# Kernel optimization log

Hardware: AMD Instinct MI355X
Metric: run time of the kernel (lower is better)

The kernel has to match this reference:

```python
import jax, jax.numpy as jnp
import numpy as np

TEMPERATURE = 0.5   # cfg.LOSS.TEMPERATURE
REG = 0.5           # Sinkhorn entropic regularization
NUM_ITER = 100      # numItermax in forward call
STOP_THR = 1e-9

BS, NUM_CLASSES, DIM = 16384, 1000, 512


def _l2norm(x):
    return x / jnp.linalg.norm(x, axis=-1, keepdims=True)


def setup_inputs() -> dict:
    key = jax.random.key(0)
    k1, k2, k3 = jax.random.split(key, 3)
    features = _l2norm(jax.random.normal(k1, (BS, DIM), jnp.float32))
    text_features = _l2norm(jax.random.normal(k2, (NUM_CLASSES, DIM), jnp.float32))
    ratios = jax.random.uniform(k3, (NUM_CLASSES,), jnp.float32)
    ratios = ratios / ratios.sum()  # class prior, sums to 1
    return {"features": features, "text_features": text_features, "ratios": ratios}


def sinkhorn_knopp(a, b, M, reg):
    """Faithful Sinkhorn-Knopp: u/v scaling loop with NaN/Inf bail-out and
    every-10-iters convergence check, unrolled as a masked lax.scan."""
    dim_a, dim_b = a.shape[0], b.shape[0]
    K = jnp.exp(M / -reg)                 # [dim_a, dim_b]
    Kp = (1.0 / a)[:, None] * K           # [dim_a, dim_b]
    u0 = jnp.ones((dim_a,), M.dtype) / dim_a
    v0 = jnp.ones((dim_b,), M.dtype) / dim_b

    def step(carry, ii):
        u, v, done = carry
        KtU = K.T @ u                     # [dim_b]
        v_new = b / KtU
        u_new = 1.0 / (Kp @ v_new)        # [dim_a]
        bad = (jnp.any(KtU == 0)
               | jnp.any(~jnp.isfinite(u_new))
               | jnp.any(~jnp.isfinite(v_new)))
        # err check (original does it when ii % 10 == 0)
        tmp2 = (u_new @ K) * v_new        # einsum('i,ij,j->j', u, K, v)
        err = jnp.linalg.norm(tmp2 - b)
        converged = ((ii % 10) == 0) & (err < STOP_THR)
        keep_prev = done | bad            # revert to uprev/vprev on bad, freeze after done
        u2 = jnp.where(keep_prev, u, u_new)
        v2 = jnp.where(keep_prev, v, v_new)
        return (u2, v2, done | bad | converged), None

    (u, v, _), _ = jax.lax.scan(step, (u0, v0, jnp.array(False)), jnp.arange(NUM_ITER))
    return u[:, None] * K * v[None, :]


def reference(features, text_features, ratios):
    sim_matrix = (features @ text_features.T) / TEMPERATURE   # [bs, C]
    cost_matrix = 1.0 - sim_matrix
    bs = features.shape[0]
    a = jnp.ones((bs,), features.dtype)       # row marginal (uniform over batch)
    b = ratios * bs                            # column marginal (class ratios)
    plan = sinkhorn_knopp(a, b, sim_matrix / cost_matrix, REG)  # [bs, C]
    return plan
```

## Files before the change

### kernel.cpp

```cpp
#include <hip/hip_runtime.h>
#include <hip/hip_bf16.h>

typedef float   f32x4_t  __attribute__((ext_vector_type(4)));
typedef float   f32x2_t  __attribute__((ext_vector_type(2)));
typedef __bf16  bf16x8_t __attribute__((ext_vector_type(8)));
typedef int     i32x4_t  __attribute__((ext_vector_type(4)));

#define N_ROWS   16384
#define N_COLS   1000
#define N_COLS_P 1024
#define N_DIM    512
#define N_ITER   100
#define PBLK     256
#define PTHR     512
#define RED0     64

__device__ __forceinline__ float ldf_sc1(const float* p) {
    return __hip_atomic_load(p, __ATOMIC_RELAXED, __HIP_MEMORY_SCOPE_AGENT);
}
__device__ __forceinline__ void stf_sc1(float* p, float v) {
    __hip_atomic_store(p, v, __ATOMIC_RELAXED, __HIP_MEMORY_SCOPE_AGENT);
}
__device__ __forceinline__ int ldi_sc1(const int* p) {
    return __hip_atomic_load(p, __ATOMIC_RELAXED, __HIP_MEMORY_SCOPE_AGENT);
}
__device__ __forceinline__ void sti_sc1(int* p, int v) {
    __hip_atomic_store(p, v, __ATOMIC_RELAXED, __HIP_MEMORY_SCOPE_AGENT);
}
__device__ __forceinline__ void st2_sc1(float* p, float a, float b) {
    const unsigned long long u =
        ((unsigned long long)__builtin_bit_cast(unsigned, b) << 32) |
        __builtin_bit_cast(unsigned, a);
    __hip_atomic_store((unsigned long long*)p, u, __ATOMIC_RELAXED,
                       __HIP_MEMORY_SCOPE_AGENT);
}

__device__ __forceinline__ unsigned short f2bf(float f) {
    unsigned int u = __builtin_bit_cast(unsigned int, f);
    u += 0x7FFFu + ((u >> 16) & 1u);
    return (unsigned short)(u >> 16);
}

__device__ __forceinline__ void gridbar(int* bar, int g) {
    __syncthreads();
    if (blockIdx.x == 0) {
        if (threadIdx.x < 64) {
            const int l = threadIdx.x;
            for (;;) {
                int ok = 1;
#pragma unroll
                for (int h = 0; h < 4; ++h) {
                    const int slot = (h << 6) + l;
                    if (slot) ok &= (ldi_sc1(bar + slot) >= g);
                }
                if (__all(ok)) break;
            }
            if (l == 0) sti_sc1(bar + 256, g);
        }
    } else {
        if (threadIdx.x == 0) {
            sti_sc1(bar + (int)blockIdx.x, g);
            while (ldi_sc1(bar + 256) < g) __builtin_amdgcn_s_sleep(2);
        }
    }
    __syncthreads();
}

template <int MODE>
__launch_bounds__(256)
__global__ void k_gemm(const float* __restrict__ F, const float* __restrict__ T,
                       void* __restrict__ Kout, float* __restrict__ cpart,
                       const float* __restrict__ v_com, const float* __restrict__ u_both,
                       const int* __restrict__ flags)
{
    __shared__ unsigned short lA[128 * 72];
    __shared__ unsigned short lB[128 * 72];
    __shared__ float cs_lds[4 * 64];

    const int bm = blockIdx.x;
    const int bn = blockIdx.y;
    const int m0 = bm << 7;
    const int n0 = bn << 7;
    const int t  = threadIdx.x;
    const int lane = t & 63;
    const int wid  = t >> 6;
    const int wr = wid >> 1;
    const int wc = wid & 1;

    f32x4_t acc[4][4];
#pragma unroll
    for (int a = 0; a < 4; ++a)
#pragma unroll
        for (int b = 0; b < 4; ++b)
            acc[a][b] = (f32x4_t){0.f, 0.f, 0.f, 0.f};

    const int srow = t >> 4;
    const int scol = (t & 15) << 2;

    for (int kt = 0; kt < N_DIM; kt += 64) {
#pragma unroll
        for (int r = 0; r < 8; ++r) {
            const int rr = srow + (r << 4);
            const float4 av = *(const float4*)(F + (size_t)(m0 + rr) * N_DIM + kt + scol);
            ushort4 a4; a4.x = f2bf(av.x); a4.y = f2bf(av.y); a4.z = f2bf(av.z); a4.w = f2bf(av.w);
            *(ushort4*)(&lA[rr * 72 + scol]) = a4;
            const int gn = n0 + rr;
            float4 bv = make_float4(0.f, 0.f, 0.f, 0.f);
            if (gn < N_COLS) bv = *(const float4*)(T + (size_t)gn * N_DIM + kt + scol);
            ushort4 b4; b4.x = f2bf(bv.x); b4.y = f2bf(bv.y); b4.z = f2bf(bv.z); b4.w = f2bf(bv.w);
            *(ushort4*)(&lB[rr * 72 + scol]) = b4;
        }
        __syncthreads();
#pragma unroll
        for (int ks = 0; ks < 2; ++ks) {
            bf16x8_t afr[4], bfr[4];
#pragma unroll
            for (int mf = 0; mf < 4; ++mf) {
                const int r = (wr << 6) + (mf << 4) + (lane & 15);
                const int off = r * 72 + (ks << 5) + ((lane >> 4) << 3);
                afr[mf] = __builtin_bit_cast(bf16x8_t, *(const i32x4_t*)(&lA[off]));
            }
#pragma unroll
            for (int nf = 0; nf < 4; ++nf) {
                const int r = (wc << 6) + (nf << 4) + (lane & 15);
                const int off = r * 72 + (ks << 5) + ((lane >> 4) << 3);
                bfr[nf] = __builtin_bit_cast(bf16x8_t, *(const i32x4_t*)(&lB[off]));
            }
#pragma unroll
            for (int mf = 0; mf < 4; ++mf)
#pragma unroll
                for (int nf = 0; nf < 4; ++nf)
                    acc[mf][nf] = __builtin_amdgcn_mfma_f32_16x16x32_bf16(
                        afr[mf], bfr[nf], acc[mf][nf], 0, 0, 0);
        }
        __syncthreads();
    }

    int usel = 2;
    if (MODE == 1) usel = flags[1];
    float csum[4] = {0.f, 0.f, 0.f, 0.f};
#pragma unroll
    for (int mf = 0; mf < 4; ++mf) {
#pragma unroll
        for (int nf = 0; nf < 4; ++nf) {
#pragma unroll
            for (int j = 0; j < 4; ++j) {
                const float d = acc[mf][nf][j];
                const float s = 2.f * d;
                const float M = s / (1.f - s);
                const float kv = __expf(-2.f * M);
                const int grow = m0 + (wr << 6) + (mf << 4) + ((lane >> 4) << 2) + j;
                const int gcol = n0 + (wc << 6) + (nf << 4) + (lane & 15);
                if (MODE == 0) {
                    ((unsigned short*)Kout)[(size_t)grow * N_COLS_P + gcol] =
                        (gcol < N_COLS) ? f2bf(kv) : (unsigned short)0;
                    csum[nf] += kv;
                } else {
                    if (gcol < N_COLS) {
                        const float u = (usel == 2) ? (1.f / 16384.f)
                                                    : u_both[(size_t)usel * N_ROWS + grow];
                        ((float*)Kout)[(size_t)grow * N_COLS + gcol] = u * kv * v_com[gcol];
                    }
                }
            }
        }
    }
    if (MODE == 0) {
#pragma unroll
        for (int nf = 0; nf < 4; ++nf) {
            csum[nf] += __shfl_xor(csum[nf], 16);
            csum[nf] += __shfl_xor(csum[nf], 32);
        }
        if (lane < 16) {
#pragma unroll
            for (int nf = 0; nf < 4; ++nf)
                cs_lds[wid * 64 + (nf << 4) + lane] = csum[nf];
        }
        __syncthreads();
        if (t < 128) {
            const int cw = t >> 6;
            const int c6 = t & 63;
            cpart[(size_t)bm * N_COLS_P + n0 + t] =
                cs_lds[cw * 64 + c6] + cs_lds[(cw + 2) * 64 + c6];
        }
    }
}

__launch_bounds__(128)
__global__ void k_init(const float* __restrict__ cpart, float* __restrict__ ktu0,
                       float* __restrict__ vcom, float* __restrict__ err2,
                       int* __restrict__ flags, int* __restrict__ bar)
{
    const int j = blockIdx.x * 128 + threadIdx.x;
    if (j < N_COLS) {
        float s = 0.f;
        for (int p = 0; p < 128; ++p) s += cpart[(size_t)p * N_COLS_P + j];
        ktu0[j] = s * (1.f / 16384.f);
        vcom[j] = 1.f / 1000.f;
    } else {
        ktu0[j] = 1.f;
        vcom[j] = 0.f;
    }
    if (j <= 256) bar[j] = 0;
    if (j < 64) err2[j] = 0.f;
    if (j == 0) { flags[0] = 0; flags[1] = 2; flags[2] = 0; flags[3] = 0; }
}

__launch_bounds__(PTHR, 2)
__global__ void k_persist(const unsigned short* __restrict__ Kb,
                          const float* __restrict__ ratios,
                          float* __restrict__ ktu,
                          float* __restrict__ utmp,
                          float* __restrict__ vcom,
                          float* __restrict__ partials,
                          float* __restrict__ err2,
                          int* __restrict__ flags,
                          int* __restrict__ bar)
{
    __shared__ float vnew[N_COLS_P];
    __shared__ float wp[8][N_COLS_P];
    __shared__ float wred[8][16];
    __shared__ float errl[16];
    __shared__ int ibc[2];
    const int t = threadIdx.x, lane = t & 63, wid = t >> 6, b = blockIdx.x;
    const int row0 = (b << 6) + (wid << 3);
    const int rb = b - RED0;
    const bool isred = (rb >= 0 && rb < 64);

    unsigned kp[8][8];
#pragma unroll
    for (int r = 0; r < 8; ++r) {
        const unsigned* rp = (const unsigned*)(Kb + (size_t)(row0 + r) * N_COLS_P);
#pragma unroll
        for (int q = 0; q < 8; ++q) kp[r][q] = rp[(q << 6) + lane];
    }
    const float bj0 = (t < N_COLS) ? ratios[t] * 16384.f : 0.f;
    const float bj1 = (t + PTHR < N_COLS) ? ratios[t + PTHR] * 16384.f : 0.f;

    int bar_g = 0;
    int usel = 2;

    for (int ii = 0; ii < N_ITER; ++ii) {
        const int p = ii & 1;
        float* __restrict__ ktu_cur = ktu + p * N_COLS_P;
        float* __restrict__ ktu_nxt = ktu + (1 - p) * N_COLS_P;

        int badl = 0;
        {
            const float v0 = bj0 / ldf_sc1(ktu_cur + t);
            const float v1 = bj1 / ldf_sc1(ktu_cur + t + PTHR);
            badl |= !isfinite(v0) | !isfinite(v1);
            vnew[t] = v0;
            vnew[t + PTHR] = v1;
        }
        __syncthreads();
        float vr[16];
#pragma unroll
        for (int q = 0; q < 8; ++q) {
            const f32x2_t vv = *(const f32x2_t*)&vnew[(q << 7) + (lane << 1)];
            vr[2*q] = vv[0]; vr[2*q+1] = vv[1];
        }
        float dots[8];
#pragma unroll
        for (int r = 0; r < 8; ++r) {
            float p0 = 0.f, p1 = 0.f, p2 = 0.f, p3 = 0.f;
#pragma unroll
            for (int q = 0; q < 8; ++q) {
                const unsigned u = kp[r][q];
                const float lo = __builtin_bit_cast(float, u << 16);
                const float hi = __builtin_bit_cast(float, u & 0xFFFF0000u);
                if (q & 1) { p2 = fmaf(lo, vr[2*q], p2); p3 = fmaf(hi, vr[2*q+1], p3); }
                else       { p0 = fmaf(lo, vr[2*q], p0); p1 = fmaf(hi, vr[2*q+1], p1); }
            }
            dots[r] = (p0 + p1) + (p2 + p3);
        }
#pragma unroll
        for (int s = 1; s <= 32; s <<= 1) {
#pragma unroll
            for (int r = 0; r < 8; ++r) dots[r] += __shfl_xor(dots[r], s);
        }
        float u8[8];
#pragma unroll
        for (int r = 0; r < 8; ++r) { u8[r] = 1.f / dots[r]; badl |= !isfinite(u8[r]); }
        if (lane == 0) {
            float* uo = utmp + (size_t)p * N_ROWS + row0;
#pragma unroll
            for (int r = 0; r < 8; ++r) uo[r] = u8[r];
        }
        if (__any(badl) && lane == 0)
            __hip_atomic_fetch_or(&flags[2], 1, __ATOMIC_RELAXED, __HIP_MEMORY_SCOPE_AGENT);

        float creg[16];
#pragma unroll
        for (int e = 0; e < 16; ++e) creg[e] = 0.f;
#pragma unroll
        for (int r = 0; r < 8; ++r) {
#pragma unroll
            for (int q = 0; q < 8; ++q) {
                const unsigned u = kp[r][q];
                const float lo = __builtin_bit_cast(float, u << 16);
                const float hi = __builtin_bit_cast(float, u & 0xFFFF0000u);
                creg[2*q]   = fmaf(lo, u8[r], creg[2*q]);
                creg[2*q+1] = fmaf(hi, u8[r], creg[2*q+1]);
            }
        }
#pragma unroll
        for (int q = 0; q < 8; ++q)
            *(f32x2_t*)&wp[wid][(q << 7) + (lane << 1)] = (f32x2_t){creg[2*q], creg[2*q+1]};
        __syncthreads();
        {
            const int j2 = t << 1;
            f32x2_t s2 = *(const f32x2_t*)&wp[0][j2];
#pragma unroll
            for (int w = 1; w < 8; ++w) {
                const f32x2_t x = *(const f32x2_t*)&wp[w][j2];
                s2[0] += x[0]; s2[1] += x[1];
            }
            st2_sc1(&partials[(size_t)b * N_COLS_P + j2], s2[0], s2[1]);
        }
        ++bar_g; gridbar(bar, bar_g);

        if (t == 0) ibc[0] = ldi_sc1(&flags[2]);
        __syncthreads();
        const int bad = ibc[0];
        float bsum = 0.f;
        if (!bad && isred) {
            const int col = (rb << 4) + (t & 15);
            const int rgrp = t >> 4;
#pragma unroll
            for (int k = 0; k < 8; ++k)
                bsum += ldf_sc1(&partials[(size_t)(rgrp + (k << 5)) * N_COLS_P + col]);
            bsum += __shfl_xor(bsum, 16);
            bsum += __shfl_xor(bsum, 32);
            if (lane < 16) wred[wid][lane] = bsum;
        }
        __syncthreads();
        if (!bad && isred && t < 16) {
            const int col = (rb << 4) + t;
            float s = 0.f;
#pragma unroll
            for (int w = 0; w < 8; ++w) s += wred[w][t];
            float errc = 0.f;
            if (col < N_COLS) {
                stf_sc1(&ktu_nxt[col], s);
                const float bj = ratios[col] * 16384.f;
                const float vn = bj / ldf_sc1(&ktu_cur[col]);
                const float d  = s * vn - bj;
                errc = d * d;
            } else {
                stf_sc1(&ktu_nxt[col], 1.f);
            }
            errl[t] = errc;
        }
        __syncthreads();
        if (!bad && isred && t == 0) {
            float e = 0.f;
#pragma unroll
            for (int i = 0; i < 16; ++i) e += errl[i];
            stf_sc1(&err2[rb], e);
        }
        ++bar_g; gridbar(bar, bar_g);

        if (bad) break;
        usel = p;
        if ((ii % 10) == 0) {
            float e = (t < 64) ? ldf_sc1(&err2[t]) : 0.f;
            if (t < 64) {
#pragma unroll
                for (int sh = 1; sh <= 32; sh <<= 1) e += __shfl_xor(e, sh);
            }
            if (t == 0) ibc[1] = (e < 1e-18f) ? 1 : 0;
            __syncthreads();
            const int conv = ibc[1];
            __syncthreads();
            if (conv) break;
        }
    }

    if (isred && t < 16 && usel != 2) {
        const int col = (rb << 4) + t;
        if (col < N_COLS)
            vcom[col] = (ratios[col] * 16384.f) /
                        ldf_sc1(&ktu[(size_t)usel * N_COLS_P + col]);
    }
    if (b == 0 && t == 0) flags[1] = usel;
}

extern "C" void kernel_launch(void* const* d_in, const int* in_sizes, int n_in,
                              void* d_out, int out_size, void* d_ws, size_t ws_size,
                              hipStream_t stream)
{
    const float* F      = (const float*)d_in[0];
    const float* T      = (const float*)d_in[1];
    const float* ratios = (const float*)d_in[2];
    float* out = (float*)d_out;
    unsigned short* Kb = (unsigned short*)d_out;

    float* ws        = (float*)d_ws;
    float* partials  = ws;
    float* ktu       = partials + (size_t)PBLK * N_COLS_P;
    float* utmp      = ktu + 2 * N_COLS_P;
    float* vcom      = utmp + 2 * N_ROWS;
    float* err2      = vcom + N_COLS_P;
    int*   flags     = (int*)(err2 + 64);
    int*   bar       = flags + 4;
    const size_t need_bytes = ((size_t)PBLK * N_COLS_P + 2 * N_COLS_P + 2 * N_ROWS +
                               N_COLS_P + 64) * sizeof(float) + (4 + 257) * sizeof(int);
    if (ws_size < need_bytes) return;

    k_gemm<0><<<dim3(128, 8), 256, 0, stream>>>(F, T, Kb, partials, nullptr, nullptr, flags);
    k_init<<<8, 128, 0, stream>>>(partials, ktu, vcom, err2, flags, bar);
    k_persist<<<PBLK, PTHR, 0, stream>>>(Kb, ratios, ktu, utmp, vcom, partials,
                                         err2, flags, bar);
    k_gemm<1><<<dim3(128, 8), 256, 0, stream>>>(F, T, out, nullptr, vcom, utmp, flags);
}
```

Baseline: 2.128 ms.

## Replace centralized grid barriers with producer/consumer ready flags in Sinkhorn loop

Result: slower. 2.245 ms (+5.5%).

```diff
diff --git a/kernel.cpp b/kernel.cpp
--- a/kernel.cpp
+++ b/kernel.cpp
@@ -13,7 +13,7 @@
 #define N_ITER   100
 #define PBLK     256
 #define PTHR     512
-#define RED0     64
+#define NRED     64
 
 __device__ __forceinline__ float ldf_sc1(const float* p) {
     return __hip_atomic_load(p, __ATOMIC_RELAXED, __HIP_MEMORY_SCOPE_AGENT);
@@ -34,36 +34,14 @@
     __hip_atomic_store((unsigned long long*)p, u, __ATOMIC_RELAXED,
                        __HIP_MEMORY_SCOPE_AGENT);
 }
+__device__ __forceinline__ void drain_vmem() {
+    asm volatile("s_waitcnt vmcnt(0)" ::: "memory");
+}
 
 __device__ __forceinline__ unsigned short f2bf(float f) {
     unsigned int u = __builtin_bit_cast(unsigned int, f);
     u += 0x7FFFu + ((u >> 16) & 1u);
     return (unsigned short)(u >> 16);
-}
-
-__device__ __forceinline__ void gridbar(int* bar, int g) {
-    __syncthreads();
-    if (blockIdx.x == 0) {
-        if (threadIdx.x < 64) {
-            const int l = threadIdx.x;
-            for (;;) {
-                int ok = 1;
-#pragma unroll
-                for (int h = 0; h < 4; ++h) {
-                    const int slot = (h << 6) + l;
-                    if (slot) ok &= (ldi_sc1(bar + slot) >= g);
-                }
-                if (__all(ok)) break;
-            }
-            if (l == 0) sti_sc1(bar + 256, g);
-        }
-    } else {
-        if (threadIdx.x == 0) {
-            sti_sc1(bar + (int)blockIdx.x, g);
-            while (ldi_sc1(bar + 256) < g) __builtin_amdgcn_s_sleep(2);
-        }
-    }
-    __syncthreads();
 }
 
 template <int MODE>
@@ -188,8 +166,9 @@
 
 __launch_bounds__(128)
 __global__ void k_init(const float* __restrict__ cpart, float* __restrict__ ktu0,
-                       float* __restrict__ vcom, float* __restrict__ err2,
-                       int* __restrict__ flags, int* __restrict__ bar)
+                       float* __restrict__ vcom, int* __restrict__ flags,
+                       int* __restrict__ pready, int* __restrict__ rready,
+                       int* __restrict__ flags2)
 {
     const int j = blockIdx.x * 128 + threadIdx.x;
     if (j < N_COLS) {
@@ -201,9 +180,10 @@
         ktu0[j] = 1.f;
         vcom[j] = 0.f;
     }
-    if (j <= 256) bar[j] = 0;
-    if (j < 64) err2[j] = 0.f;
-    if (j == 0) { flags[0] = 0; flags[1] = 2; flags[2] = 0; flags[3] = 0; }
+    if (j < PBLK) pready[j] = 0;
+    if (j < NRED) rready[j] = 0;
+    if (j < 128)  flags2[j] = 0;
+    if (j < 4)    flags[j] = (j == 1) ? 2 : 0;
 }
 
 __launch_bounds__(PTHR, 2)
@@ -213,19 +193,19 @@
                           float* __restrict__ utmp,
                           float* __restrict__ vcom,
                           float* __restrict__ partials,
-                          float* __restrict__ err2,
                           int* __restrict__ flags,
-                          int* __restrict__ bar)
+                          int* __restrict__ pready,
+                          int* __restrict__ rready,
+                          int* __restrict__ flags2)
 {
-    __shared__ float vnew[N_COLS_P];
+    __shared__ float vbuf[2][N_COLS_P];
     __shared__ float wp[8][N_COLS_P];
-    __shared__ float wred[8][16];
-    __shared__ float errl[16];
-    __shared__ int ibc[2];
+    __shared__ float redw[8][16];
+    __shared__ float rbc;
+    __shared__ int ibc;
     const int t = threadIdx.x, lane = t & 63, wid = t >> 6, b = blockIdx.x;
     const int row0 = (b << 6) + (wid << 3);
-    const int rb = b - RED0;
-    const bool isred = (rb >= 0 && rb < 64);
+    const bool isred = (b < NRED);
 
     unsigned kp[8][8];
 #pragma unroll
@@ -237,27 +217,62 @@
     const float bj0 = (t < N_COLS) ? ratios[t] * 16384.f : 0.f;
     const float bj1 = (t + PTHR < N_COLS) ? ratios[t + PTHR] * 16384.f : 0.f;
 
-    int bar_g = 0;
     int usel = 2;
 
-    for (int ii = 0; ii < N_ITER; ++ii) {
+    for (int ii = 0; ii <= N_ITER; ++ii) {
         const int p = ii & 1;
-        float* __restrict__ ktu_cur = ktu + p * N_COLS_P;
-        float* __restrict__ ktu_nxt = ktu + (1 - p) * N_COLS_P;
-
-        int badl = 0;
-        {
-            const float v0 = bj0 / ldf_sc1(ktu_cur + t);
-            const float v1 = bj1 / ldf_sc1(ktu_cur + t + PTHR);
-            badl |= !isfinite(v0) | !isfinite(v1);
-            vnew[t] = v0;
-            vnew[t + PTHR] = v1;
-        }
-        __syncthreads();
+        float kc0, kc1;
+
+        if (ii > 0) {
+            if (wid == 0) {
+                for (;;) {
+                    const int ok = (ldi_sc1(&rready[lane]) >= ii);
+                    if (__all(ok)) break;
+                    __builtin_amdgcn_s_sleep(1);
+                }
+            }
+            __syncthreads();
+            if (t == 0) ibc = ldi_sc1(&flags2[ii - 1]);
+            __syncthreads();
+            if (ibc) break;
+            usel = (ii - 1) & 1;
+            kc0 = ldf_sc1(&ktu[(p << 10) + t]);
+            kc1 = ldf_sc1(&ktu[(p << 10) + t + PTHR]);
+            if (((ii - 1) % 10) == 0) {
+                const float vo0 = vbuf[usel][t], vo1 = vbuf[usel][t + PTHR];
+                const float d0 = (t < N_COLS) ? kc0 * vo0 - bj0 : 0.f;
+                const float d1 = (t + PTHR < N_COLS) ? kc1 * vo1 - bj1 : 0.f;
+                float e = d0 * d0 + d1 * d1;
+#pragma unroll
+                for (int sh = 1; sh <= 32; sh <<= 1) e += __shfl_xor(e, sh);
+                if (lane == 0) redw[wid][0] = e;
+                __syncthreads();
+                if (t == 0) {
+                    float s = 0.f;
+#pragma unroll
+                    for (int w = 0; w < 8; ++w) s += redw[w][0];
+                    rbc = s;
+                }
+                __syncthreads();
+                if (rbc < 1e-18f) break;
+            }
+            if (ii == N_ITER) break;
+        } else {
+            kc0 = ldf_sc1(&ktu[t]);
+            kc1 = ldf_sc1(&ktu[t + PTHR]);
+        }
+
+        const float v0 = bj0 / kc0;
+        const float v1 = bj1 / kc1;
+        const int badv = (kc0 == 0.f) | (kc1 == 0.f) | (!isfinite(v0)) | (!isfinite(v1));
+        vbuf[p][t] = v0;
+        vbuf[p][t + PTHR] = v1;
+        if (__syncthreads_or(badv)) break;
+
         float vr[16];
 #pragma unroll
         for (int q = 0; q < 8; ++q) {
-            const f32x2_t vv = *(const f32x2_t*)&vnew[(q << 7) + (lane << 1)];
+            const f32x2_t vv = *(const f32x2_t*)&vbuf[p][(q << 7) + (lane << 1)];
             vr[2*q] = vv[0]; vr[2*q+1] = vv[1];
         }
         float dots[8];
@@ -280,15 +295,17 @@
             for (int r = 0; r < 8; ++r) dots[r] += __shfl_xor(dots[r], s);
         }
         float u8[8];
-#pragma unroll
-        for (int r = 0; r < 8; ++r) { u8[r] = 1.f / dots[r]; badl |= !isfinite(u8[r]); }
+        int ubad = 0;
+#pragma unroll
+        for (int r = 0; r < 8; ++r) { u8[r] = 1.f / dots[r]; ubad |= !isfinite(u8[r]); }
         if (lane == 0) {
-            float* uo = utmp + (size_t)p * N_ROWS + row0;
+            float* uo = utmp + ((size_t)p << 14) + row0;
 #pragma unroll
             for (int r = 0; r < 8; ++r) uo[r] = u8[r];
         }
-        if (__any(badl) && lane == 0)
-            __hip_atomic_fetch_or(&flags[2], 1, __ATOMIC_RELAXED, __HIP_MEMORY_SCOPE_AGENT);
+        if (__any(ubad) && lane == 0)
+            __hip_atomic_fetch_or(&flags2[ii], 1, __ATOMIC_RELAXED,
+                                  __HIP_MEMORY_SCOPE_AGENT);
 
         float creg[16];
 #pragma unroll
@@ -316,74 +333,54 @@
                 const f32x2_t x = *(const f32x2_t*)&wp[w][j2];
                 s2[0] += x[0]; s2[1] += x[1];
             }
-            st2_sc1(&partials[(size_t)b * N_COLS_P + j2], s2[0], s2[1]);
-        }
-        ++bar_g; gridbar(bar, bar_g);
-
-        if (t == 0) ibc[0] = ldi_sc1(&flags[2]);
+            st2_sc1(&partials[((size_t)b << 10) + j2], s2[0], s2[1]);
+        }
+        drain_vmem();
         __syncthreads();
-        const int bad = ibc[0];
-        float bsum = 0.f;
-        if (!bad && isred) {
-            const int col = (rb << 4) + (t & 15);
-            const int rgrp = t >> 4;
+        if (t == 0) sti_sc1(&pready[b], ii + 1);
+
+        if (isred) {
+            if (wid == 0) {
+                for (;;) {
+                    int ok = 1;
+#pragma unroll
+                    for (int h = 0; h < 4; ++h)
+                        ok &= (ldi_sc1(&pready[(h << 6) + lane]) >= ii + 1);
+                    if (__all(ok)) break;
+                }
+            }
+            __syncthreads();
+            const int col = (b << 4) + (t & 15);
+            const int pr0 = t >> 4;
+            float s = 0.f;
 #pragma unroll
             for (int k = 0; k < 8; ++k)
-                bsum += ldf_sc1(&partials[(size_t)(rgrp + (k << 5)) * N_COLS_P + col]);
-            bsum += __shfl_xor(bsum, 16);
-            bsum += __shfl_xor(bsum, 32);
-            if (lane < 16) wred[wid][lane] = bsum;
-        }
-        __syncthreads();
-        if (!bad && isred && t < 16) {
-            const int col = (rb << 4) + t;
-            float s = 0.f;
-#pragma unroll
-            for (int w = 0; w < 8; ++w) s += wred[w][t];
-            float errc = 0.f;
-            if (col < N_COLS) {
-                stf_sc1(&ktu_nxt[col], s);
-                const float bj = ratios[col] * 16384.f;
-                const float vn = bj / ldf_sc1(&ktu_cur[col]);
-                const float d  = s * vn - bj;
-                errc = d * d;
-            } else {
-                stf_sc1(&ktu_nxt[col], 1.f);
-            }
-            errl[t] = errc;
-        }
-        __syncthreads();
-        if (!bad && isred && t == 0) {
-            float e = 0.f;
-#pragma unroll
-            for (int i = 0; i < 16; ++i) e += errl[i];
-            stf_sc1(&err2[rb], e);
-        }
-        ++bar_g; gridbar(bar, bar_g);
-
-        if (bad) break;
-        usel = p;
-        if ((ii % 10) == 0) {
-            float e = (t < 64) ? ldf_sc1(&err2[t]) : 0.f;
-            if (t < 64) {
-#pragma unroll
-                for (int sh = 1; sh <= 32; sh <<= 1) e += __shfl_xor(e, sh);
-            }
-            if (t == 0) ibc[1] = (e < 1e-18f) ? 1 : 0;
+                s += ldf_sc1(&partials[((size_t)(pr0 + (k << 5)) << 10) + col]);
+            s += __shfl_xor(s, 16);
+            s += __shfl_xor(s, 32);
+            if (lane < 16) redw[wid][lane] = s;
             __syncthreads();
-            const int conv = ibc[1];
+            if (t < 16) {
+                float s2 = 0.f;
+#pragma unroll
+                for (int w = 0; w < 8; ++w) s2 += redw[w][t];
+                const int c = (b << 4) + t;
+                stf_sc1(&ktu[(((ii + 1) & 1) << 10) + c], (c < N_COLS) ? s2 : 1.f);
+            }
+            drain_vmem();
             __syncthreads();
-            if (conv) break;
-        }
-    }
-
-    if (isred && t < 16 && usel != 2) {
-        const int col = (rb << 4) + t;
-        if (col < N_COLS)
-            vcom[col] = (ratios[col] * 16384.f) /
-                        ldf_sc1(&ktu[(size_t)usel * N_COLS_P + col]);
-    }
-    if (b == 0 && t == 0) flags[1] = usel;
+            if (t == 0) sti_sc1(&rready[b], ii + 1);
+        }
+    }
+
+    if (b == 0) {
+        float vf0, vf1;
+        if (usel == 2) { vf0 = 1.f / 1000.f; vf1 = 1.f / 1000.f; }
+        else           { vf0 = vbuf[usel][t]; vf1 = vbuf[usel][t + PTHR]; }
+        if (t < N_COLS) vcom[t] = vf0;
+        if (t + PTHR < N_COLS) vcom[t + PTHR] = vf1;
+        if (t == 0) flags[1] = usel;
+    }
 }
 
 extern "C" void kernel_launch(void* const* d_in, const int* in_sizes, int n_in,
@@ -401,16 +398,18 @@
     float* ktu       = partials + (size_t)PBLK * N_COLS_P;
     float* utmp      = ktu + 2 * N_COLS_P;
     float* vcom      = utmp + 2 * N_ROWS;
-    float* err2      = vcom + N_COLS_P;
-    int*   flags     = (int*)(err2 + 64);
-    int*   bar       = flags + 4;
+    int*   flags     = (int*)(vcom + N_COLS_P);
+    int*   pready    = flags + 4;
+    int*   rready    = pready + PBLK;
+    int*   flags2    = rready + NRED;
     const size_t need_bytes = ((size_t)PBLK * N_COLS_P + 2 * N_COLS_P + 2 * N_ROWS +
-                               N_COLS_P + 64) * sizeof(float) + (4 + 257) * sizeof(int);
+                               N_COLS_P) * sizeof(float) +
+                              (4 + PBLK + NRED + 128) * sizeof(int);
     if (ws_size < need_bytes) return;
 
     k_gemm<0><<<dim3(128, 8), 256, 0, stream>>>(F, T, Kb, partials, nullptr, nullptr, flags);
-    k_init<<<8, 128, 0, stream>>>(partials, ktu, vcom, err2, flags, bar);
+    k_init<<<8, 128, 0, stream>>>(partials, ktu, vcom, flags, pready, rready, flags2);
     k_persist<<<PBLK, PTHR, 0, stream>>>(Kb, ratios, ktu, utmp, vcom, partials,
-                                         err2, flags, bar);
+                                         flags, pready, rready, flags2);
     k_gemm<1><<<dim3(128, 8), 256, 0, stream>>>(F, T, out, nullptr, vcom, utmp, flags);
 }
```
